# Performance work log

Measured on AMD Instinct MI355X. Metric: run time of the kernel, lower is better.

Reference implementation:

```python
import jax, jax.numpy as jnp
import numpy as np

NUM_LAYERS = 32
HIDDEN_DIM = 2048
RANK = 64
BATCH = 2048


def setup_inputs() -> dict:
    key = jax.random.key(0)
    k_z, k_id, k_u, k_v = jax.random.split(key, 4)
    z = jax.random.normal(k_z, (BATCH, HIDDEN_DIM), dtype=jnp.float32)
    layer_ids = jax.random.randint(k_id, (BATCH,), 0, NUM_LAYERS)
    u = jax.random.normal(k_u, (NUM_LAYERS, HIDDEN_DIM, RANK), dtype=jnp.float32) * 0.01
    v = jax.random.normal(k_v, (NUM_LAYERS, HIDDEN_DIM, RANK), dtype=jnp.float32) * 0.01
    return {"z": z, "layer_ids": layer_ids, "u": u, "v": v}


def reference(z, layer_ids, u, v):
    # Gather per-sample low-rank factors: [B, H, R]
    u_g = u[layer_ids]
    v_g = v[layer_ids]
    # proj = V_l^T z : [B, R]
    proj = jnp.einsum('bhr,bh->br', v_g, z)
    # delta = U_l proj : [B, H]
    delta = jnp.einsum('bhr,br->bh', u_g, proj)
    return z + delta
```

## Files before the change

kernel.cpp:

```cpp
#include <hip/hip_runtime.h>

#define NUM_LAYERS 32
#define HIDDEN 2048
#define RANK 64
#define BATCH 2048
#define KC 256
#define HCH 256
#define MB 32
#define SCG 2
#define ZPAD 264
#define VPAD 264
#define UPAD 72
#define PPAD 72

typedef __attribute__((ext_vector_type(8))) short bf16x8;
typedef __attribute__((ext_vector_type(4))) float f32x4;

static __device__ __forceinline__ ushort f2bf(float x) {
    unsigned b = __builtin_bit_cast(unsigned, x);
    b += 0x7fffu + ((b >> 16) & 1u);
    return (ushort)(b >> 16);
}
static __device__ __forceinline__ ushort4 pack4(float4 v) {
    ushort4 r; r.x = f2bf(v.x); r.y = f2bf(v.y); r.z = f2bf(v.z); r.w = f2bf(v.w);
    return r;
}

__global__ __launch_bounds__(256)
void k_bucket_zero(const int* __restrict__ ids, float* __restrict__ proj,
                   int* __restrict__ counts, int* __restrict__ offsets,
                   int* __restrict__ perm)
{
    if (blockIdx.x == 0) {
        __shared__ int cnt[NUM_LAYERS];
        __shared__ int off[NUM_LAYERS];
        __shared__ int cur[NUM_LAYERS];
        const int t = threadIdx.x;
        if (t < NUM_LAYERS) cnt[t] = 0;
        __syncthreads();
        for (int i = t; i < BATCH; i += 256) atomicAdd(&cnt[ids[i]], 1);
        __syncthreads();
        if (t == 0) {
            int a = 0;
            for (int l = 0; l < NUM_LAYERS; ++l) { off[l] = a; a += cnt[l]; }
        }
        __syncthreads();
        if (t < NUM_LAYERS) { cur[t] = 0; counts[t] = cnt[t]; offsets[t] = off[t]; }
        __syncthreads();
        for (int i = t; i < BATCH; i += 256) {
            int l = ids[i];
            int p = off[l] + atomicAdd(&cur[l], 1);
            perm[p] = i;
        }
    } else {
        const int base = (blockIdx.x - 1) * (BATCH * RANK / 64);
        for (int i = threadIdx.x; i < BATCH * RANK / 64; i += 256)
            proj[base + i] = 0.0f;
    }
}

__global__ __launch_bounds__(256)
void k_proj(const float* __restrict__ z, const float* __restrict__ v,
            const int* __restrict__ counts, const int* __restrict__ offsets,
            const int* __restrict__ perm, float* __restrict__ proj)
{
    const int kc = blockIdx.x, l = blockIdx.y, sc = blockIdx.z;
    const int n = counts[l], o = offsets[l];
    if (sc * MB >= n) return;
    const int t = threadIdx.x;
    const int w = t >> 6, lane = t & 63;
    const int m16 = lane & 15, quad = lane >> 4;
    const int kbase = kc * KC;

    __shared__ ushort vt[RANK * VPAD];
    __shared__ ushort zt[MB * ZPAD];
    __shared__ int    bidx[MB];

    #pragma unroll
    for (int it = 0; it < 16; ++it) {
        const int idx = it * 256 + t;
        const int hh = idx >> 4, rq = idx & 15;
        const float4 uv = *(const float4*)
            &v[((size_t)l * HIDDEN + kbase + hh) * RANK + rq * 4];
        vt[(rq * 4 + 0) * VPAD + hh] = f2bf(uv.x);
        vt[(rq * 4 + 1) * VPAD + hh] = f2bf(uv.y);
        vt[(rq * 4 + 2) * VPAD + hh] = f2bf(uv.z);
        vt[(rq * 4 + 3) * VPAD + hh] = f2bf(uv.w);
    }

    for (int base = sc * MB; base < n; base += SCG * MB) {
        const int nb = (n - base < MB) ? (n - base) : MB;
        __syncthreads();
        if (t < MB) bidx[t] = (t < nb) ? perm[o + base + t] : 0;
        __syncthreads();
        #pragma unroll
        for (int it = 0; it < 8; ++it) {
            const int idx = it * 256 + t;
            const int si = idx >> 6, q = idx & 63;
            float4 zv = make_float4(0.f, 0.f, 0.f, 0.f);
            if (si < nb)
                zv = *(const float4*)&z[(size_t)bidx[si] * HIDDEN + kbase + q * 4];
            *(ushort4*)&zt[si * ZPAD + q * 4] = pack4(zv);
        }
        __syncthreads();

        f32x4 acc0 = {0.f, 0.f, 0.f, 0.f}, acc1 = {0.f, 0.f, 0.f, 0.f};
        #pragma unroll
        for (int kt = 0; kt < 8; ++kt) {
            const int koff = kt * 32 + quad * 8;
            const bf16x8 bf = *(const bf16x8*)&vt[(w * 16 + m16) * VPAD + koff];
            const bf16x8 a0 = *(const bf16x8*)&zt[m16 * ZPAD + koff];
            const bf16x8 a1 = *(const bf16x8*)&zt[(16 + m16) * ZPAD + koff];
            acc0 = __builtin_amdgcn_mfma_f32_16x16x32_bf16(a0, bf, acc0, 0, 0, 0);
            acc1 = __builtin_amdgcn_mfma_f32_16x16x32_bf16(a1, bf, acc1, 0, 0, 0);
        }
        const int r = w * 16 + m16;
        #pragma unroll
        for (int reg = 0; reg < 4; ++reg) {
            const int row = quad * 4 + reg;
            if (row < nb)
                atomicAdd(&proj[(size_t)bidx[row] * RANK + r], acc0[reg]);
            if (16 + row < nb)
                atomicAdd(&proj[(size_t)bidx[16 + row] * RANK + r], acc1[reg]);
        }
    }
}

__global__ __launch_bounds__(256)
void k_delta(const float* __restrict__ z, const float* __restrict__ u,
             const int* __restrict__ counts, const int* __restrict__ offsets,
             const int* __restrict__ perm, const float* __restrict__ proj,
             float* __restrict__ out)
{
    const int hc = blockIdx.x, l = blockIdx.y, sc = blockIdx.z;
    const int n = counts[l], o = offsets[l];
    if (sc * MB >= n) return;
    const int t = threadIdx.x;
    const int w = t >> 6, lane = t & 63;
    const int m16 = lane & 15, quad = lane >> 4;
    const int hbase = hc * HCH;

    __shared__ ushort ut[HCH * UPAD];
    __shared__ ushort pt[MB * PPAD];
    __shared__ int    bidx[MB];

    #pragma unroll
    for (int it = 0; it < 16; ++it) {
        const int idx = it * 256 + t;
        const int hh = idx >> 4, rq = idx & 15;
        const float4 uv = *(const float4*)
            &u[((size_t)l * HIDDEN + hbase + hh) * RANK + rq * 4];
        *(ushort4*)&ut[hh * UPAD + rq * 4] = pack4(uv);
    }

    for (int base = sc * MB; base < n; base += SCG * MB) {
        const int nb = (n - base < MB) ? (n - base) : MB;
        __syncthreads();
        if (t < MB) bidx[t] = (t < nb) ? perm[o + base + t] : 0;
        __syncthreads();
        #pragma unroll
        for (int it = 0; it < 2; ++it) {
            const int idx = it * 256 + t;
            const int si = idx >> 4, rq = idx & 15;
            float4 pv = make_float4(0.f, 0.f, 0.f, 0.f);
            if (si < nb)
                pv = *(const float4*)&proj[(size_t)bidx[si] * RANK + rq * 4];
            *(ushort4*)&pt[si * PPAD + rq * 4] = pack4(pv);
        }
        __syncthreads();

        f32x4 acc[2][4];
        #pragma unroll
        for (int mt = 0; mt < 2; ++mt)
            #pragma unroll
            for (int nt = 0; nt < 4; ++nt)
                acc[mt][nt] = (f32x4){0.f, 0.f, 0.f, 0.f};

        #pragma unroll
        for (int kt = 0; kt < 2; ++kt) {
            const int koff = kt * 32 + quad * 8;
            const bf16x8 a0 = *(const bf16x8*)&pt[m16 * PPAD + koff];
            const bf16x8 a1 = *(const bf16x8*)&pt[(16 + m16) * PPAD + koff];
            #pragma unroll
            for (int nt = 0; nt < 4; ++nt) {
                const int h = (w * 4 + nt) * 16 + m16;
                const bf16x8 bf = *(const bf16x8*)&ut[h * UPAD + koff];
                acc[0][nt] = __builtin_amdgcn_mfma_f32_16x16x32_bf16(a0, bf, acc[0][nt], 0, 0, 0);
                acc[1][nt] = __builtin_amdgcn_mfma_f32_16x16x32_bf16(a1, bf, acc[1][nt], 0, 0, 0);
            }
        }
        #pragma unroll
        for (int mt = 0; mt < 2; ++mt) {
            #pragma unroll
            for (int reg = 0; reg < 4; ++reg) {
                const int si = mt * 16 + quad * 4 + reg;
                if (si < nb) {
                    const size_t rowb = (size_t)bidx[si] * HIDDEN + hbase;
                    #pragma unroll
                    for (int nt = 0; nt < 4; ++nt) {
                        const int h = (w * 4 + nt) * 16 + m16;
                        out[rowb + h] = z[rowb + h] + acc[mt][nt][reg];
                    }
                }
            }
        }
    }
}

extern "C" void kernel_launch(void* const* d_in, const int* in_sizes, int n_in,
                              void* d_out, int out_size, void* d_ws, size_t ws_size,
                              hipStream_t stream)
{
    const float* z   = (const float*)d_in[0];
    const int*   ids = (const int*)d_in[1];
    const float* u   = (const float*)d_in[2];
    const float* v   = (const float*)d_in[3];
    float* out = (float*)d_out;

    float* proj   = (float*)d_ws;
    int* counts   = (int*)(proj + (size_t)BATCH * RANK);
    int* offsets  = counts + NUM_LAYERS;
    int* perm     = offsets + NUM_LAYERS;

    hipLaunchKernelGGL(k_bucket_zero, dim3(65), dim3(256), 0, stream,
                       ids, proj, counts, offsets, perm);
    hipLaunchKernelGGL(k_proj, dim3(HIDDEN / KC, NUM_LAYERS, SCG), dim3(256), 0, stream,
                       z, v, counts, offsets, perm, proj);
    hipLaunchKernelGGL(k_delta, dim3(HIDDEN / HCH, NUM_LAYERS, SCG), dim3(256), 0, stream,
                       z, u, counts, offsets, perm, proj, out);
}
```

Measured before the change: 111.0 us.

## Fuse projection and delta into one kernel with pre-converted bf16 weights

Adds a prep kernel that converts U and V to bf16 once, storing V transposed, alongside the layer bucketing. A single fused kernel then computes proj for a tile of 8 samples over all hidden chunks, keeps it in shared memory, and immediately applies U to write the output. This removes the proj atomics, the proj zeroing, and one kernel launch. In exchange, each block re-reads the full bf16 V and U of its layer for every 8-sample tile, and only half of each 16-row MFMA tile carries real samples.

```diff
diff --git a/kernel.cpp b/kernel.cpp
--- a/kernel.cpp
+++ b/kernel.cpp
@@ -4,14 +4,15 @@
 #define HIDDEN 2048
 #define RANK 64
 #define BATCH 2048
-#define KC 256
-#define HCH 256
-#define MB 32
-#define SCG 2
+#define CHK 256
+#define NCHK (HIDDEN / CHK)
+#define SB 8
+#define NSC 16
+#define VPAD 264
 #define ZPAD 264
-#define VPAD 264
 #define UPAD 72
 #define PPAD 72
+#define PREPPAD 264
 
 typedef __attribute__((ext_vector_type(8))) short bf16x8;
 typedef __attribute__((ext_vector_type(4))) float f32x4;
@@ -26,16 +27,52 @@
     return r;
 }
 
+
 __global__ __launch_bounds__(256)
-void k_bucket_zero(const int* __restrict__ ids, float* __restrict__ proj,
-                   int* __restrict__ counts, int* __restrict__ offsets,
-                   int* __restrict__ perm)
+void k_prep(const float* __restrict__ v, const float* __restrict__ u,
+            const int* __restrict__ ids,
+            ushort* __restrict__ vbf, ushort* __restrict__ ubf,
+            int* __restrict__ counts, int* __restrict__ offsets,
+            int* __restrict__ perm)
 {
-    if (blockIdx.x == 0) {
+    const int b = blockIdx.x, t = threadIdx.x;
+    if (b < 256) {
+        const int l = b >> 3, kbase = (b & 7) * CHK;
+        __shared__ ushort vtile[RANK * PREPPAD];
+        #pragma unroll
+        for (int it = 0; it < 16; ++it) {
+            const int idx = it * 256 + t;
+            const int hh = idx >> 4, rq = idx & 15;
+            const float4 f = *(const float4*)
+                &v[((size_t)l * HIDDEN + kbase + hh) * RANK + rq * 4];
+            vtile[(rq * 4 + 0) * PREPPAD + hh] = f2bf(f.x);
+            vtile[(rq * 4 + 1) * PREPPAD + hh] = f2bf(f.y);
+            vtile[(rq * 4 + 2) * PREPPAD + hh] = f2bf(f.z);
+            vtile[(rq * 4 + 3) * PREPPAD + hh] = f2bf(f.w);
+        }
+        __syncthreads();
+        #pragma unroll
+        for (int it = 0; it < 8; ++it) {
+            const int idx = it * 256 + t;
+            const int r = idx >> 5, c = idx & 31;
+            const bf16x8 d = *(const bf16x8*)&vtile[r * PREPPAD + c * 8];
+            *(bf16x8*)&vbf[((size_t)l * RANK + r) * HIDDEN + kbase + c * 8] = d;
+        }
+    } else if (b < 512) {
+        const int bb = b - 256;
+        const int l = bb >> 3, hbase = (bb & 7) * CHK;
+        #pragma unroll
+        for (int it = 0; it < 16; ++it) {
+            const int idx = it * 256 + t;
+            const int hh = idx >> 4, rq = idx & 15;
+            const size_t off = ((size_t)l * HIDDEN + hbase + hh) * RANK + rq * 4;
+            const float4 f = *(const float4*)&u[off];
+            *(ushort4*)&ubf[off] = pack4(f);
+        }
+    } else {
         __shared__ int cnt[NUM_LAYERS];
         __shared__ int off[NUM_LAYERS];
         __shared__ int cur[NUM_LAYERS];
-        const int t = threadIdx.x;
         if (t < NUM_LAYERS) cnt[t] = 0;
         __syncthreads();
         for (int i = t; i < BATCH; i += 256) atomicAdd(&cnt[ids[i]], 1);
@@ -52,154 +89,105 @@
             int p = off[l] + atomicAdd(&cur[l], 1);
             perm[p] = i;
         }
-    } else {
-        const int base = (blockIdx.x - 1) * (BATCH * RANK / 64);
-        for (int i = threadIdx.x; i < BATCH * RANK / 64; i += 256)
-            proj[base + i] = 0.0f;
     }
 }
 
 __global__ __launch_bounds__(256)
-void k_proj(const float* __restrict__ z, const float* __restrict__ v,
-            const int* __restrict__ counts, const int* __restrict__ offsets,
-            const int* __restrict__ perm, float* __restrict__ proj)
+void k_fused(const float* __restrict__ z,
+             const ushort* __restrict__ vbf, const ushort* __restrict__ ubf,
+             const int* __restrict__ counts, const int* __restrict__ offsets,
+             const int* __restrict__ perm, float* __restrict__ out)
 {
-    const int kc = blockIdx.x, l = blockIdx.y, sc = blockIdx.z;
+    const int sc = blockIdx.x, l = blockIdx.y;
     const int n = counts[l], o = offsets[l];
-    if (sc * MB >= n) return;
     const int t = threadIdx.x;
     const int w = t >> 6, lane = t & 63;
     const int m16 = lane & 15, quad = lane >> 4;
-    const int kbase = kc * KC;
-
-    __shared__ ushort vt[RANK * VPAD];
-    __shared__ ushort zt[MB * ZPAD];
-    __shared__ int    bidx[MB];
-
-    #pragma unroll
-    for (int it = 0; it < 16; ++it) {
-        const int idx = it * 256 + t;
-        const int hh = idx >> 4, rq = idx & 15;
-        const float4 uv = *(const float4*)
-            &v[((size_t)l * HIDDEN + kbase + hh) * RANK + rq * 4];
-        vt[(rq * 4 + 0) * VPAD + hh] = f2bf(uv.x);
-        vt[(rq * 4 + 1) * VPAD + hh] = f2bf(uv.y);
-        vt[(rq * 4 + 2) * VPAD + hh] = f2bf(uv.z);
-        vt[(rq * 4 + 3) * VPAD + hh] = f2bf(uv.w);
-    }
-
-    for (int base = sc * MB; base < n; base += SCG * MB) {
-        const int nb = (n - base < MB) ? (n - base) : MB;
-        __syncthreads();
-        if (t < MB) bidx[t] = (t < nb) ? perm[o + base + t] : 0;
-        __syncthreads();
-        #pragma unroll
-        for (int it = 0; it < 8; ++it) {
-            const int idx = it * 256 + t;
-            const int si = idx >> 6, q = idx & 63;
-            float4 zv = make_float4(0.f, 0.f, 0.f, 0.f);
-            if (si < nb)
-                zv = *(const float4*)&z[(size_t)bidx[si] * HIDDEN + kbase + q * 4];
-            *(ushort4*)&zt[si * ZPAD + q * 4] = pack4(zv);
-        }
-        __syncthreads();
-
-        f32x4 acc0 = {0.f, 0.f, 0.f, 0.f}, acc1 = {0.f, 0.f, 0.f, 0.f};
-        #pragma unroll
-        for (int kt = 0; kt < 8; ++kt) {
-            const int koff = kt * 32 + quad * 8;
-            const bf16x8 bf = *(const bf16x8*)&vt[(w * 16 + m16) * VPAD + koff];
-            const bf16x8 a0 = *(const bf16x8*)&zt[m16 * ZPAD + koff];
-            const bf16x8 a1 = *(const bf16x8*)&zt[(16 + m16) * ZPAD + koff];
-            acc0 = __builtin_amdgcn_mfma_f32_16x16x32_bf16(a0, bf, acc0, 0, 0, 0);
-            acc1 = __builtin_amdgcn_mfma_f32_16x16x32_bf16(a1, bf, acc1, 0, 0, 0);
-        }
-        const int r = w * 16 + m16;
-        #pragma unroll
-        for (int reg = 0; reg < 4; ++reg) {
-            const int row = quad * 4 + reg;
-            if (row < nb)
-                atomicAdd(&proj[(size_t)bidx[row] * RANK + r], acc0[reg]);
-            if (16 + row < nb)
-                atomicAdd(&proj[(size_t)bidx[16 + row] * RANK + r], acc1[reg]);
-        }
-    }
-}
-
-__global__ __launch_bounds__(256)
-void k_delta(const float* __restrict__ z, const float* __restrict__ u,
-             const int* __restrict__ counts, const int* __restrict__ offsets,
-             const int* __restrict__ perm, const float* __restrict__ proj,
-             float* __restrict__ out)
-{
-    const int hc = blockIdx.x, l = blockIdx.y, sc = blockIdx.z;
-    const int n = counts[l], o = offsets[l];
-    if (sc * MB >= n) return;
-    const int t = threadIdx.x;
-    const int w = t >> 6, lane = t & 63;
-    const int m16 = lane & 15, quad = lane >> 4;
-    const int hbase = hc * HCH;
-
-    __shared__ ushort ut[HCH * UPAD];
-    __shared__ ushort pt[MB * PPAD];
-    __shared__ int    bidx[MB];
-
-    #pragma unroll
-    for (int it = 0; it < 16; ++it) {
-        const int idx = it * 256 + t;
-        const int hh = idx >> 4, rq = idx & 15;
-        const float4 uv = *(const float4*)
-            &u[((size_t)l * HIDDEN + hbase + hh) * RANK + rq * 4];
-        *(ushort4*)&ut[hh * UPAD + rq * 4] = pack4(uv);
-    }
-
-    for (int base = sc * MB; base < n; base += SCG * MB) {
-        const int nb = (n - base < MB) ? (n - base) : MB;
-        __syncthreads();
-        if (t < MB) bidx[t] = (t < nb) ? perm[o + base + t] : 0;
-        __syncthreads();
-        #pragma unroll
-        for (int it = 0; it < 2; ++it) {
-            const int idx = it * 256 + t;
-            const int si = idx >> 4, rq = idx & 15;
-            float4 pv = make_float4(0.f, 0.f, 0.f, 0.f);
-            if (si < nb)
-                pv = *(const float4*)&proj[(size_t)bidx[si] * RANK + rq * 4];
-            *(ushort4*)&pt[si * PPAD + rq * 4] = pack4(pv);
-        }
-        __syncthreads();
-
-        f32x4 acc[2][4];
-        #pragma unroll
-        for (int mt = 0; mt < 2; ++mt)
-            #pragma unroll
-            for (int nt = 0; nt < 4; ++nt)
-                acc[mt][nt] = (f32x4){0.f, 0.f, 0.f, 0.f};
-
-        #pragma unroll
-        for (int kt = 0; kt < 2; ++kt) {
-            const int koff = kt * 32 + quad * 8;
-            const bf16x8 a0 = *(const bf16x8*)&pt[m16 * PPAD + koff];
-            const bf16x8 a1 = *(const bf16x8*)&pt[(16 + m16) * PPAD + koff];
+
+    __shared__ ushort smem[RANK * VPAD + 16 * ZPAD];
+    __shared__ ushort pt[16 * PPAD];
+    __shared__ int bidx[SB];
+    ushort* vt = smem;
+    ushort* zt = smem + RANK * VPAD;
+    ushort* ut = smem;
+
+    for (int base = sc * SB; base < n; base += NSC * SB) {
+        const int nb = (n - base < SB) ? (n - base) : SB;
+        __syncthreads();
+        if (t < SB) bidx[t] = (t < nb) ? perm[o + base + t] : 0;
+
+        f32x4 acc = {0.f, 0.f, 0.f, 0.f};
+        for (int kc = 0; kc < NCHK; ++kc) {
+            const int kbase = kc * CHK;
+            __syncthreads();
+            #pragma unroll
+            for (int it = 0; it < 8; ++it) {
+                const int idx = it * 256 + t;
+                const int r = idx >> 5, c = idx & 31;
+                const bf16x8 d = *(const bf16x8*)
+                    &vbf[((size_t)l * RANK + r) * HIDDEN + kbase + c * 8];
+                *(bf16x8*)&vt[r * VPAD + c * 8] = d;
+            }
+            #pragma unroll
+            for (int it = 0; it < 2; ++it) {
+                const int idx = it * 256 + t;
+                const int si = idx >> 6, q = idx & 63;
+                if (si < nb) {
+                    const float4 f = *(const float4*)
+                        &z[(size_t)bidx[si] * HIDDEN + kbase + q * 4];
+                    *(ushort4*)&zt[si * ZPAD + q * 4] = pack4(f);
+                }
+            }
+            __syncthreads();
+            #pragma unroll
+            for (int kt = 0; kt < 8; ++kt) {
+                const int koff = kt * 32 + quad * 8;
+                const bf16x8 a  = *(const bf16x8*)&zt[m16 * ZPAD + koff];
+                const bf16x8 bm = *(const bf16x8*)&vt[(w * 16 + m16) * VPAD + koff];
+                acc = __builtin_amdgcn_mfma_f32_16x16x32_bf16(a, bm, acc, 0, 0, 0);
+            }
+        }
+        #pragma unroll
+        for (int reg = 0; reg < 4; ++reg)
+            pt[(quad * 4 + reg) * PPAD + w * 16 + m16] = f2bf(acc[reg]);
+        __syncthreads();
+
+        const bf16x8 pa0 = *(const bf16x8*)&pt[m16 * PPAD + quad * 8];
+        const bf16x8 pa1 = *(const bf16x8*)&pt[m16 * PPAD + 32 + quad * 8];
+
+        for (int hc = 0; hc < NCHK; ++hc) {
+            const int hbase = hc * CHK;
+            if (hc) __syncthreads();
+            #pragma unroll
+            for (int it = 0; it < 8; ++it) {
+                const int idx = it * 256 + t;
+                const int hh = idx >> 3, rq = idx & 7;
+                const bf16x8 d = *(const bf16x8*)
+                    &ubf[((size_t)l * HIDDEN + hbase + hh) * RANK + rq * 8];
+                *(bf16x8*)&ut[hh * UPAD + rq * 8] = d;
+            }
+            __syncthreads();
+
+            f32x4 acc2[4];
+            #pragma unroll
+            for (int nt = 0; nt < 4; ++nt) acc2[nt] = (f32x4){0.f, 0.f, 0.f, 0.f};
             #pragma unroll
             for (int nt = 0; nt < 4; ++nt) {
-                const int h = (w * 4 + nt) * 16 + m16;
-                const bf16x8 bf = *(const bf16x8*)&ut[h * UPAD + koff];
-                acc[0][nt] = __builtin_amdgcn_mfma_f32_16x16x32_bf16(a0, bf, acc[0][nt], 0, 0, 0);
-                acc[1][nt] = __builtin_amdgcn_mfma_f32_16x16x32_bf16(a1, bf, acc[1][nt], 0, 0, 0);
-            }
-        }
-        #pragma unroll
-        for (int mt = 0; mt < 2; ++mt) {
+                const int hcol = (w * 4 + nt) * 16 + m16;
+                const bf16x8 b0 = *(const bf16x8*)&ut[hcol * UPAD + quad * 8];
+                const bf16x8 b1 = *(const bf16x8*)&ut[hcol * UPAD + 32 + quad * 8];
+                acc2[nt] = __builtin_amdgcn_mfma_f32_16x16x32_bf16(pa0, b0, acc2[nt], 0, 0, 0);
+                acc2[nt] = __builtin_amdgcn_mfma_f32_16x16x32_bf16(pa1, b1, acc2[nt], 0, 0, 0);
+            }
             #pragma unroll
             for (int reg = 0; reg < 4; ++reg) {
-                const int si = mt * 16 + quad * 4 + reg;
+                const int si = quad * 4 + reg;
                 if (si < nb) {
                     const size_t rowb = (size_t)bidx[si] * HIDDEN + hbase;
                     #pragma unroll
                     for (int nt = 0; nt < 4; ++nt) {
-                        const int h = (w * 4 + nt) * 16 + m16;
-                        out[rowb + h] = z[rowb + h] + acc[mt][nt][reg];
+                        const int hcol = (w * 4 + nt) * 16 + m16;
+                        out[rowb + hcol] = z[rowb + hcol] + acc2[nt][reg];
                     }
                 }
             }
@@ -217,15 +205,14 @@
     const float* v   = (const float*)d_in[3];
     float* out = (float*)d_out;
 
-    float* proj   = (float*)d_ws;
-    int* counts   = (int*)(proj + (size_t)BATCH * RANK);
-    int* offsets  = counts + NUM_LAYERS;
-    int* perm     = offsets + NUM_LAYERS;
-
-    hipLaunchKernelGGL(k_bucket_zero, dim3(65), dim3(256), 0, stream,
-                       ids, proj, counts, offsets, perm);
-    hipLaunchKernelGGL(k_proj, dim3(HIDDEN / KC, NUM_LAYERS, SCG), dim3(256), 0, stream,
-                       z, v, counts, offsets, perm, proj);
-    hipLaunchKernelGGL(k_delta, dim3(HIDDEN / HCH, NUM_LAYERS, SCG), dim3(256), 0, stream,
-                       z, u, counts, offsets, perm, proj, out);
-}
+    ushort* vbf  = (ushort*)d_ws;
+    ushort* ubf  = vbf + (size_t)NUM_LAYERS * RANK * HIDDEN;
+    int* counts  = (int*)(ubf + (size_t)NUM_LAYERS * HIDDEN * RANK);
+    int* offsets = counts + NUM_LAYERS;
+    int* perm    = offsets + NUM_LAYERS;
+
+    hipLaunchKernelGGL(k_prep, dim3(513), dim3(256), 0, stream,
+                       v, u, ids, vbf, ubf, counts, offsets, perm);
+    hipLaunchKernelGGL(k_fused, dim3(NSC, NUM_LAYERS), dim3(256), 0, stream,
+                       z, vbf, ubf, counts, offsets, perm, out);
+}
```

Result: slower. 138.0 us (+24.4%).
